# Kernel tuning notes

Measured on AMD Instinct MI355X. Metric: run time of the kernel, lower is better.

## Reference

```python
import jax, jax.numpy as jnp
import numpy as np
from jax import lax

BATCH = 4096
SEQ = 200
VOCAB = 100000
HID = 128


def setup_inputs() -> dict:
    key = jax.random.key(0)
    k0, k1, k2, k3, k4 = jax.random.split(key, 5)
    inputs = jax.random.randint(k0, (BATCH, SEQ), 0, VOCAB, dtype=jnp.int32).astype(jnp.int64)
    emb = jax.random.normal(k1, (VOCAB, HID), dtype=jnp.float32) * 0.05
    # Keras GRU (reset_after=True): kernel [H,3H], recurrent_kernel [H,3H], bias [2,3H]
    kernel = jax.random.normal(k2, (HID, 3 * HID), dtype=jnp.float32) * (1.0 / np.sqrt(HID))
    rec_kernel = jax.random.normal(k3, (HID, 3 * HID), dtype=jnp.float32) * (1.0 / np.sqrt(HID))
    bias = jax.random.normal(k4, (2, 3 * HID), dtype=jnp.float32) * 0.01
    return {"inputs": inputs, "emb": emb, "kernel": kernel, "rec_kernel": rec_kernel, "bias": bias}


def _masked_gru(x, mask, kernel, rec_kernel, bias):
    # x: [B,S,H] embedded inputs; mask: [B,S] bool (True = valid timestep)
    input_bias, rec_bias = bias[0], bias[1]
    # Precompute all input projections in one big GEMM: [B,S,3H]
    xproj = jnp.einsum('bsh,hk->bsk', x, kernel) + input_bias
    B, H = x.shape[0], x.shape[2]

    def step(h, scan_in):
        xp, m = scan_in  # xp: [B,3H], m: [B]
        hp = h @ rec_kernel + rec_bias  # [B,3H]
        xz, xr, xh = xp[:, :H], xp[:, H:2 * H], xp[:, 2 * H:]
        hz, hr, hh_rec = hp[:, :H], hp[:, H:2 * H], hp[:, 2 * H:]
        z = jax.nn.sigmoid(xz + hz)
        r = jax.nn.sigmoid(xr + hr)
        hh = jnp.tanh(xh + r * hh_rec)  # reset_after=True: r applied after recurrent matmul
        h_new = z * h + (1.0 - z) * hh
        # mask_zero semantics: masked steps carry previous state through
        h_new = jnp.where(m[:, None], h_new, h)
        return h_new, None

    h0 = jnp.zeros((B, H), dtype=x.dtype)
    xs = (jnp.swapaxes(xproj, 0, 1), jnp.swapaxes(mask, 0, 1))  # time-major
    h_final, _ = lax.scan(step, h0, xs)
    return h_final  # [B,H] == last valid-step output under Keras masking


def reference(inputs, emb, kernel, rec_kernel, bias):
    x = emb[inputs]              # [B,S,H] embedding lookup
    mask = inputs != 0           # mask_zero=True
    return _masked_gru(x, mask, kernel, rec_kernel, bias)
```

## Files before the change

kernel.cpp:

```cpp
#include <hip/hip_runtime.h>

#define BATCH 4096
#define SEQ   200
#define HID   128
#define ROWS  16
#define NTH   512

typedef _Float16 f16;
typedef f16 f16x4 __attribute__((ext_vector_type(4)));
typedef f16 f16x8 __attribute__((ext_vector_type(8)));
typedef float f32x4 __attribute__((ext_vector_type(4)));

#define MFMA(a, b, c) __builtin_amdgcn_mfma_f32_16x16x32_f16((a), (b), (c), 0, 0, 0)

__device__ __forceinline__ float fast_exp2(float x) {
#if defined(__has_builtin) && __has_builtin(__builtin_amdgcn_exp2f)
    return __builtin_amdgcn_exp2f(x);
#else
    float r; asm volatile("v_exp_f32 %0, %1\n\ts_nop 0" : "=v"(r) : "v"(x)); return r;
#endif
}
__device__ __forceinline__ float fast_rcp(float x) {
#if defined(__has_builtin) && __has_builtin(__builtin_amdgcn_rcpf)
    return __builtin_amdgcn_rcpf(x);
#else
    float r; asm volatile("v_rcp_f32 %0, %1\n\ts_nop 0" : "=v"(r) : "v"(x)); return r;
#endif
}
#define LOG2E  1.442695041f
#define LOG2E2 2.885390082f

__global__ __attribute__((amdgpu_flat_work_group_size(NTH, NTH)))
void gru_mfma(const int* __restrict__ inputs,
              const float* __restrict__ emb,
              const float* __restrict__ kernel,
              const float* __restrict__ rec_kernel,
              const float* __restrict__ bias,
              float* __restrict__ out)
{
    __shared__ __align__(16) f16 xb[3][4][64][8];
    __shared__ __align__(16) f16 hb[2][4][64][8];
    __shared__ int tok_sh[2][ROWS];
    __shared__ int ts_sh;

    const int tid  = threadIdx.x;
    const int lane = tid & 63;
    const int j0   = (tid >> 6) * 16;
    const int l15  = lane & 15;
    const int hi   = lane >> 4;
    const int r0   = hi * 4;
    const int row0 = blockIdx.x * ROWS;

    if (tid == 0) { int any = 0; for (int i = 1; i < 128; i += 2) any |= inputs[i]; ts_sh = any ? 1 : 2; }

    f16x8 Bx[3][4];
    f16x8 Brz[4], Brr[4], Brh[4];
    const float gsc[3] = { -LOG2E, -LOG2E, LOG2E2 };
#pragma unroll
    for (int g = 0; g < 3; ++g)
#pragma unroll
        for (int kt = 0; kt < 4; ++kt) {
            f16x8 t;
#pragma unroll
            for (int e = 0; e < 8; ++e)
                t[e] = (f16)(gsc[g] * kernel[(size_t)(kt * 32 + hi * 8 + e) * 384 + g * HID + j0 + l15]);
            Bx[g][kt] = t;
        }
#pragma unroll
    for (int kt = 0; kt < 4; ++kt) {
        f16x8 tz, tr, th;
#pragma unroll
        for (int e = 0; e < 8; ++e) {
            const size_t krow = (size_t)(kt * 32 + hi * 8 + e) * 384;
            tz[e] = (f16)(-LOG2E  * rec_kernel[krow + j0 + l15]);
            tr[e] = (f16)(-LOG2E  * rec_kernel[krow + HID + j0 + l15]);
            th[e] = (f16)(LOG2E2 * rec_kernel[krow + 2 * HID + j0 + l15]);
        }
        Brz[kt] = tz; Brr[kt] = tr; Brh[kt] = th;
    }

    f32x4 bzv, brv, bxhv, brhv;
#pragma unroll
    for (int i = 0; i < 4; ++i) {
        const int c = j0 + r0 + i;
        bzv[i]  = -LOG2E * (bias[c]       + bias[384 + c]);
        brv[i]  = -LOG2E * (bias[128 + c] + bias[512 + c]);
        bxhv[i] =  LOG2E2 * bias[256 + c];
        brhv[i] =  LOG2E2 * bias[640 + c];
    }

    f32x4 h = {0.f, 0.f, 0.f, 0.f};

    const int hk  = j0 + r0;
    const int hwi = (((hk >> 5) * 64) + (((hk & 31) >> 3) * 16) + l15) * 8 + (hk & 7);

    const int skt  = tid >> 7;
    const int sidx = tid & 127;
    const int su   = sidx >> 1;
    const int shalf= sidx & 1;
    const int sb   = su & 15;
    const int shid = skt * 32 + (su >> 4) * 8 + shalf * 4;
    const int sw   = (skt * 64 + su) * 8 + shalf * 4;
    const bool twr = (tid < 32) && ((tid & 1) == 0);

    for (int i = tid; i < 4 * 64 * 8; i += NTH) ((f16*)hb)[i] = (f16)0.f;
    __syncthreads();
    const int ts = ts_sh;

    const size_t tbase = (size_t)(row0 + sb) * SEQ;
    const int tok0 = inputs[(tbase + 0) * ts];
    int t1 = inputs[(tbase + 1) * ts];
    int t2 = inputs[(tbase + 2) * ts];
    if (twr) tok_sh[0][sb] = tok0;
    {
        const float4 v0 = *(const float4*)&emb[(size_t)tok0 * HID + shid];
        const float4 v1 = *(const float4*)&emb[(size_t)t1   * HID + shid];
        f16x4 a; a[0] = (f16)v0.x; a[1] = (f16)v0.y; a[2] = (f16)v0.z; a[3] = (f16)v0.w;
        f16x4 b; b[0] = (f16)v1.x; b[1] = (f16)v1.y; b[2] = (f16)v1.z; b[3] = (f16)v1.w;
        *(f16x4*)&((f16*)xb)[sw] = a;
        *(f16x4*)&((f16*)xb)[1 * (4 * 64 * 8) + sw] = b;
    }
    __syncthreads();

    f32x4 azx = bzv, arx = brv, axc = bxhv;
#pragma unroll
    for (int kt = 0; kt < 4; ++kt) {
        const f16x8 xB = *(const f16x8*)&xb[0][kt][lane][0];
        azx = MFMA(Bx[0][kt], xB, azx);
        arx = MFMA(Bx[1][kt], xB, arx);
        axc = MFMA(Bx[2][kt], xB, axc);
    }

    int rd_x = 1, wr_x = 2;
    for (int s = 0; s < SEQ; ++s) {
        const int cur = s & 1, nxt = cur ^ 1;
        const bool pf1 = (s + 1 < SEQ);
        const bool pf2 = (s + 2 < SEQ);
        float4 pv; int t3 = t2;
        if (pf2) {
            pv = *(const float4*)&emb[(size_t)t2 * HID + shid];
            const int s3 = (s + 3 < SEQ) ? (s + 3) : (SEQ - 1);
            t3 = inputs[(tbase + s3) * ts];
        }

        const int tkk = tok_sh[cur][l15];

        f32x4 az = azx, ar = arx, ah = brhv;
#pragma unroll
        for (int kt = 0; kt < 4; ++kt) {
            const f16x8 hB = *(const f16x8*)&hb[cur][kt][lane][0];
            az = MFMA(Brz[kt], hB, az);
            ar = MFMA(Brr[kt], hB, ar);
            ah = MFMA(Brh[kt], hB, ah);
        }

        f16x4 hv;
#pragma unroll
        for (int i = 0; i < 4; ++i) {
            const float z  = fast_rcp(1.f + fast_exp2(az[i]));
            const float rg = fast_rcp(1.f + fast_exp2(ar[i]));
            const float u  = axc[i] + rg * ah[i];
            const float hh = 1.f - 2.f * fast_rcp(1.f + fast_exp2(u));
            const float hn = hh + z * (h[i] - hh);
            h[i] = (tkk != 0) ? hn : h[i];
            hv[i] = (f16)h[i];
        }

        *(f16x4*)&((f16*)hb)[nxt * (4 * 64 * 8) + hwi] = hv;

        if (pf1) {
            azx = bzv; arx = brv; axc = bxhv;
#pragma unroll
            for (int kt = 0; kt < 4; ++kt) {
                const f16x8 xB = *(const f16x8*)&xb[rd_x][kt][lane][0];
                azx = MFMA(Bx[0][kt], xB, azx);
                arx = MFMA(Bx[1][kt], xB, arx);
                axc = MFMA(Bx[2][kt], xB, axc);
            }
            if (twr) tok_sh[nxt][sb] = t1;
        }
        if (pf2) {
            f16x4 xv; xv[0] = (f16)pv.x; xv[1] = (f16)pv.y; xv[2] = (f16)pv.z; xv[3] = (f16)pv.w;
            *(f16x4*)&((f16*)xb)[wr_x * (4 * 64 * 8) + sw] = xv;
        }
        t1 = t2; t2 = t3;
        rd_x = (rd_x == 2) ? 0 : rd_x + 1;
        wr_x = (wr_x == 2) ? 0 : wr_x + 1;
        __syncthreads();
    }

    float4 o; o.x = h[0]; o.y = h[1]; o.z = h[2]; o.w = h[3];
    *(float4*)&out[(size_t)(row0 + l15) * HID + j0 + r0] = o;
}

extern "C" void kernel_launch(void* const* d_in, const int* in_sizes, int n_in,
                              void* d_out, int out_size, void* d_ws, size_t ws_size,
                              hipStream_t stream) {
    const int* inputs      = (const int*)d_in[0];
    const float* emb       = (const float*)d_in[1];
    const float* kernel    = (const float*)d_in[2];
    const float* rec_k     = (const float*)d_in[3];
    const float* bias      = (const float*)d_in[4];
    float* out             = (float*)d_out;
    gru_mfma<<<BATCH / ROWS, NTH, 0, stream>>>(inputs, emb, kernel, rec_k, bias, out);
}
```

Before: 166.7 us.

## Split input projection and recurrence into producer/consumer wave groups

Doubles the block to 1024 threads. Eight waves compute the next step's input projections and embedding prefetch into a shared-memory staging buffer, while the other eight waves run the recurrent matmul and gate math. This takes the input-projection MFMAs off the serial recurrence path. In exchange it adds shared-memory traffic for the projections, relies on matching barrier counts across divergent branches, and uses more registers and waves per block.

```diff
diff --git a/kernel.cpp b/kernel.cpp
--- a/kernel.cpp
+++ b/kernel.cpp
@@ -4,7 +4,7 @@
 #define SEQ   200
 #define HID   128
 #define ROWS  16
-#define NTH   512
+#define NTH   1024
 
 typedef _Float16 f16;
 typedef f16 f16x4 __attribute__((ext_vector_type(4)));
@@ -40,12 +40,16 @@
 {
     __shared__ __align__(16) f16 xb[3][4][64][8];
     __shared__ __align__(16) f16 hb[2][4][64][8];
+    __shared__ __align__(16) float xp[2][3][8][64][4];
     __shared__ int tok_sh[2][ROWS];
     __shared__ int ts_sh;
 
     const int tid  = threadIdx.x;
     const int lane = tid & 63;
-    const int j0   = (tid >> 6) * 16;
+    const int wv   = tid >> 6;
+    const bool isX = (wv < 8);
+    const int w    = isX ? wv : (wv - 8);
+    const int j0   = w * 16;
     const int l15  = lane & 15;
     const int hi   = lane >> 4;
     const int r0   = hi * 4;
@@ -53,144 +57,162 @@
 
     if (tid == 0) { int any = 0; for (int i = 1; i < 128; i += 2) any |= inputs[i]; ts_sh = any ? 1 : 2; }
 
-    f16x8 Bx[3][4];
-    f16x8 Brz[4], Brr[4], Brh[4];
-    const float gsc[3] = { -LOG2E, -LOG2E, LOG2E2 };
-#pragma unroll
-    for (int g = 0; g < 3; ++g)
-#pragma unroll
-        for (int kt = 0; kt < 4; ++kt) {
-            f16x8 t;
-#pragma unroll
-            for (int e = 0; e < 8; ++e)
-                t[e] = (f16)(gsc[g] * kernel[(size_t)(kt * 32 + hi * 8 + e) * 384 + g * HID + j0 + l15]);
-            Bx[g][kt] = t;
-        }
-#pragma unroll
-    for (int kt = 0; kt < 4; ++kt) {
-        f16x8 tz, tr, th;
-#pragma unroll
-        for (int e = 0; e < 8; ++e) {
-            const size_t krow = (size_t)(kt * 32 + hi * 8 + e) * 384;
-            tz[e] = (f16)(-LOG2E  * rec_kernel[krow + j0 + l15]);
-            tr[e] = (f16)(-LOG2E  * rec_kernel[krow + HID + j0 + l15]);
-            th[e] = (f16)(LOG2E2 * rec_kernel[krow + 2 * HID + j0 + l15]);
-        }
-        Brz[kt] = tz; Brr[kt] = tr; Brh[kt] = th;
-    }
-
-    f32x4 bzv, brv, bxhv, brhv;
-#pragma unroll
-    for (int i = 0; i < 4; ++i) {
-        const int c = j0 + r0 + i;
-        bzv[i]  = -LOG2E * (bias[c]       + bias[384 + c]);
-        brv[i]  = -LOG2E * (bias[128 + c] + bias[512 + c]);
-        bxhv[i] =  LOG2E2 * bias[256 + c];
-        brhv[i] =  LOG2E2 * bias[640 + c];
-    }
-
-    f32x4 h = {0.f, 0.f, 0.f, 0.f};
-
-    const int hk  = j0 + r0;
-    const int hwi = (((hk >> 5) * 64) + (((hk & 31) >> 3) * 16) + l15) * 8 + (hk & 7);
-
-    const int skt  = tid >> 7;
-    const int sidx = tid & 127;
-    const int su   = sidx >> 1;
-    const int shalf= sidx & 1;
-    const int sb   = su & 15;
-    const int shid = skt * 32 + (su >> 4) * 8 + shalf * 4;
-    const int sw   = (skt * 64 + su) * 8 + shalf * 4;
-    const bool twr = (tid < 32) && ((tid & 1) == 0);
-
     for (int i = tid; i < 4 * 64 * 8; i += NTH) ((f16*)hb)[i] = (f16)0.f;
     __syncthreads();
     const int ts = ts_sh;
 
-    const size_t tbase = (size_t)(row0 + sb) * SEQ;
-    const int tok0 = inputs[(tbase + 0) * ts];
-    int t1 = inputs[(tbase + 1) * ts];
-    int t2 = inputs[(tbase + 2) * ts];
-    if (twr) tok_sh[0][sb] = tok0;
-    {
-        const float4 v0 = *(const float4*)&emb[(size_t)tok0 * HID + shid];
-        const float4 v1 = *(const float4*)&emb[(size_t)t1   * HID + shid];
-        f16x4 a; a[0] = (f16)v0.x; a[1] = (f16)v0.y; a[2] = (f16)v0.z; a[3] = (f16)v0.w;
-        f16x4 b; b[0] = (f16)v1.x; b[1] = (f16)v1.y; b[2] = (f16)v1.z; b[3] = (f16)v1.w;
-        *(f16x4*)&((f16*)xb)[sw] = a;
-        *(f16x4*)&((f16*)xb)[1 * (4 * 64 * 8) + sw] = b;
-    }
-    __syncthreads();
-
-    f32x4 azx = bzv, arx = brv, axc = bxhv;
-#pragma unroll
-    for (int kt = 0; kt < 4; ++kt) {
-        const f16x8 xB = *(const f16x8*)&xb[0][kt][lane][0];
-        azx = MFMA(Bx[0][kt], xB, azx);
-        arx = MFMA(Bx[1][kt], xB, arx);
-        axc = MFMA(Bx[2][kt], xB, axc);
-    }
-
-    int rd_x = 1, wr_x = 2;
-    for (int s = 0; s < SEQ; ++s) {
-        const int cur = s & 1, nxt = cur ^ 1;
-        const bool pf1 = (s + 1 < SEQ);
-        const bool pf2 = (s + 2 < SEQ);
-        float4 pv; int t3 = t2;
-        if (pf2) {
-            pv = *(const float4*)&emb[(size_t)t2 * HID + shid];
-            const int s3 = (s + 3 < SEQ) ? (s + 3) : (SEQ - 1);
-            t3 = inputs[(tbase + s3) * ts];
-        }
-
-        const int tkk = tok_sh[cur][l15];
-
-        f32x4 az = azx, ar = arx, ah = brhv;
-#pragma unroll
-        for (int kt = 0; kt < 4; ++kt) {
-            const f16x8 hB = *(const f16x8*)&hb[cur][kt][lane][0];
-            az = MFMA(Brz[kt], hB, az);
-            ar = MFMA(Brr[kt], hB, ar);
-            ah = MFMA(Brh[kt], hB, ah);
-        }
-
-        f16x4 hv;
+    if (isX) {
+        f16x8 Bx[3][4];
+        const float gsc[3] = { -LOG2E, -LOG2E, LOG2E2 };
+#pragma unroll
+        for (int g = 0; g < 3; ++g)
+#pragma unroll
+            for (int kt = 0; kt < 4; ++kt) {
+                f16x8 t;
+#pragma unroll
+                for (int e = 0; e < 8; ++e)
+                    t[e] = (f16)(gsc[g] * kernel[(size_t)(kt * 32 + hi * 8 + e) * 384 + g * HID + j0 + l15]);
+                Bx[g][kt] = t;
+            }
+        f32x4 bzv, brv, bxhv;
 #pragma unroll
         for (int i = 0; i < 4; ++i) {
-            const float z  = fast_rcp(1.f + fast_exp2(az[i]));
-            const float rg = fast_rcp(1.f + fast_exp2(ar[i]));
-            const float u  = axc[i] + rg * ah[i];
-            const float hh = 1.f - 2.f * fast_rcp(1.f + fast_exp2(u));
-            const float hn = hh + z * (h[i] - hh);
-            h[i] = (tkk != 0) ? hn : h[i];
-            hv[i] = (f16)h[i];
-        }
-
-        *(f16x4*)&((f16*)hb)[nxt * (4 * 64 * 8) + hwi] = hv;
-
-        if (pf1) {
-            azx = bzv; arx = brv; axc = bxhv;
+            const int c = j0 + r0 + i;
+            bzv[i]  = -LOG2E * (bias[c]       + bias[384 + c]);
+            brv[i]  = -LOG2E * (bias[128 + c] + bias[512 + c]);
+            bxhv[i] =  LOG2E2 * bias[256 + c];
+        }
+
+        const int skt   = (tid >> 7) & 3;
+        const int sidx  = tid & 127;
+        const int su    = sidx >> 1;
+        const int shalf = sidx & 1;
+        const int sb    = su & 15;
+        const int shid  = skt * 32 + (su >> 4) * 8 + shalf * 4;
+        const int sw    = (skt * 64 + su) * 8 + shalf * 4;
+        const bool twr  = (tid < 32) && ((tid & 1) == 0);
+
+        const size_t tbase = (size_t)(row0 + sb) * SEQ;
+        const int tok0 = inputs[(tbase + 0) * ts];
+        int t1 = inputs[(tbase + 1) * ts];
+        int t2 = inputs[(tbase + 2) * ts];
+        if (twr) tok_sh[0][sb] = tok0;
+        {
+            const float4 v0 = *(const float4*)&emb[(size_t)tok0 * HID + shid];
+            const float4 v1 = *(const float4*)&emb[(size_t)t1   * HID + shid];
+            f16x4 a; a[0] = (f16)v0.x; a[1] = (f16)v0.y; a[2] = (f16)v0.z; a[3] = (f16)v0.w;
+            f16x4 b; b[0] = (f16)v1.x; b[1] = (f16)v1.y; b[2] = (f16)v1.z; b[3] = (f16)v1.w;
+            *(f16x4*)&((f16*)xb)[sw] = a;
+            *(f16x4*)&((f16*)xb)[1 * (4 * 64 * 8) + sw] = b;
+        }
+        __syncthreads();
+
+        {
+            f32x4 azx = bzv, arx = brv, axc = bxhv;
 #pragma unroll
             for (int kt = 0; kt < 4; ++kt) {
-                const f16x8 xB = *(const f16x8*)&xb[rd_x][kt][lane][0];
+                const f16x8 xB = *(const f16x8*)&xb[0][kt][lane][0];
                 azx = MFMA(Bx[0][kt], xB, azx);
                 arx = MFMA(Bx[1][kt], xB, arx);
                 axc = MFMA(Bx[2][kt], xB, axc);
             }
-            if (twr) tok_sh[nxt][sb] = t1;
-        }
-        if (pf2) {
-            f16x4 xv; xv[0] = (f16)pv.x; xv[1] = (f16)pv.y; xv[2] = (f16)pv.z; xv[3] = (f16)pv.w;
-            *(f16x4*)&((f16*)xb)[wr_x * (4 * 64 * 8) + sw] = xv;
-        }
-        t1 = t2; t2 = t3;
-        rd_x = (rd_x == 2) ? 0 : rd_x + 1;
-        wr_x = (wr_x == 2) ? 0 : wr_x + 1;
-        __syncthreads();
+            *(f32x4*)&xp[0][0][w][lane][0] = azx;
+            *(f32x4*)&xp[0][1][w][lane][0] = arx;
+            *(f32x4*)&xp[0][2][w][lane][0] = axc;
+        }
+        __syncthreads();
+
+        int rd_x = 1, wr_x = 2;
+        for (int s = 0; s < SEQ; ++s) {
+            const int nxt = (s & 1) ^ 1;
+            const bool pf1 = (s + 1 < SEQ);
+            const bool pf2 = (s + 2 < SEQ);
+            float4 pv; int t3 = t2;
+            if (pf2) {
+                pv = *(const float4*)&emb[(size_t)t2 * HID + shid];
+                const int s3 = (s + 3 < SEQ) ? (s + 3) : (SEQ - 1);
+                t3 = inputs[(tbase + s3) * ts];
+            }
+            if (pf1) {
+                f32x4 azx = bzv, arx = brv, axc = bxhv;
+#pragma unroll
+                for (int kt = 0; kt < 4; ++kt) {
+                    const f16x8 xB = *(const f16x8*)&xb[rd_x][kt][lane][0];
+                    azx = MFMA(Bx[0][kt], xB, azx);
+                    arx = MFMA(Bx[1][kt], xB, arx);
+                    axc = MFMA(Bx[2][kt], xB, axc);
+                }
+                *(f32x4*)&xp[nxt][0][w][lane][0] = azx;
+                *(f32x4*)&xp[nxt][1][w][lane][0] = arx;
+                *(f32x4*)&xp[nxt][2][w][lane][0] = axc;
+                if (twr) tok_sh[nxt][sb] = t1;
+            }
+            if (pf2) {
+                f16x4 xv; xv[0] = (f16)pv.x; xv[1] = (f16)pv.y; xv[2] = (f16)pv.z; xv[3] = (f16)pv.w;
+                *(f16x4*)&((f16*)xb)[wr_x * (4 * 64 * 8) + sw] = xv;
+            }
+            t1 = t2; t2 = t3;
+            rd_x = (rd_x == 2) ? 0 : rd_x + 1;
+            wr_x = (wr_x == 2) ? 0 : wr_x + 1;
+            __syncthreads();
+        }
+    } else {
+        f16x8 Brz[4], Brr[4], Brh[4];
+#pragma unroll
+        for (int kt = 0; kt < 4; ++kt) {
+            f16x8 tz, tr, th;
+#pragma unroll
+            for (int e = 0; e < 8; ++e) {
+                const size_t krow = (size_t)(kt * 32 + hi * 8 + e) * 384;
+                tz[e] = (f16)(-LOG2E  * rec_kernel[krow + j0 + l15]);
+                tr[e] = (f16)(-LOG2E  * rec_kernel[krow + HID + j0 + l15]);
+                th[e] = (f16)(LOG2E2 * rec_kernel[krow + 2 * HID + j0 + l15]);
+            }
+            Brz[kt] = tz; Brr[kt] = tr; Brh[kt] = th;
+        }
+        f32x4 brhv;
+#pragma unroll
+        for (int i = 0; i < 4; ++i) brhv[i] = LOG2E2 * bias[640 + j0 + r0 + i];
+
+        f32x4 h = {0.f, 0.f, 0.f, 0.f};
+        const int hk  = j0 + r0;
+        const int hwi = (((hk >> 5) * 64) + (((hk & 31) >> 3) * 16) + l15) * 8 + (hk & 7);
+
+        __syncthreads();
+        __syncthreads();
+
+        for (int s = 0; s < SEQ; ++s) {
+            const int cur = s & 1, nxt = cur ^ 1;
+            f32x4 az  = *(const f32x4*)&xp[cur][0][w][lane][0];
+            f32x4 ar  = *(const f32x4*)&xp[cur][1][w][lane][0];
+            const f32x4 axc = *(const f32x4*)&xp[cur][2][w][lane][0];
+            f32x4 ah  = brhv;
+            const int tkk = tok_sh[cur][l15];
+#pragma unroll
+            for (int kt = 0; kt < 4; ++kt) {
+                const f16x8 hB = *(const f16x8*)&hb[cur][kt][lane][0];
+                az = MFMA(Brz[kt], hB, az);
+                ar = MFMA(Brr[kt], hB, ar);
+                ah = MFMA(Brh[kt], hB, ah);
+            }
+            f16x4 hv;
+#pragma unroll
+            for (int i = 0; i < 4; ++i) {
+                const float z  = fast_rcp(1.f + fast_exp2(az[i]));
+                const float rg = fast_rcp(1.f + fast_exp2(ar[i]));
+                const float u  = axc[i] + rg * ah[i];
+                const float hh = 1.f - 2.f * fast_rcp(1.f + fast_exp2(u));
+                const float hn = hh + z * (h[i] - hh);
+                h[i] = (tkk != 0) ? hn : h[i];
+                hv[i] = (f16)h[i];
+            }
+            *(f16x4*)&((f16*)hb)[nxt * (4 * 64 * 8) + hwi] = hv;
+            __syncthreads();
+        }
+
+        float4 o; o.x = h[0]; o.y = h[1]; o.z = h[2]; o.w = h[3];
+        *(float4*)&out[(size_t)(row0 + l15) * HID + j0 + r0] = o;
     }
-
-    float4 o; o.x = h[0]; o.y = h[1]; o.z = h[2]; o.w = h[3];
-    *(float4*)&out[(size_t)(row0 + l15) * HID + j0 + r0] = o;
 }
 
 extern "C" void kernel_launch(void* const* d_in, const int* in_sizes, int n_in,
```

New measurement: 184.5 us. 1.11x slower.
